# Performance work log

Hardware: AMD Instinct MI355X
Metric: run time of the kernel (lower is better)

The kernel has to match this reference:

```python
import jax, jax.numpy as jnp
import numpy as np

EMBED_DIM = 1024
NUM_HEADS = 16
HEAD_DIM = EMBED_DIM // NUM_HEADS
KERNEL = 3
PAD = KERNEL // 2
B, L = 4, 1024


def conv1d(x, w, b):
    # x: [B, D, L], w: [D_out, D_in, K], b: [D_out]; 'same' padding like nn.Conv1d(padding=K//2)
    y = jax.lax.conv_general_dilated(
        x, w, window_strides=(1,), padding=[(PAD, PAD)],
        dimension_numbers=('NCH', 'OIH', 'NCH'))
    return y + b[None, :, None]


def setup_inputs() -> dict:
    key = jax.random.key(0)
    ks = jax.random.split(key, 12)
    fan = EMBED_DIM * KERNEL
    bound = 1.0 / np.sqrt(fan)
    def wconv(k):
        return jax.random.uniform(k, (EMBED_DIM, EMBED_DIM, KERNEL), jnp.float32, -bound, bound)
    def bconv(k):
        return jax.random.uniform(k, (EMBED_DIM,), jnp.float32, -bound, bound)
    return {
        'query': jax.random.normal(ks[0], (B, L, EMBED_DIM), jnp.float32),
        'key': jax.random.normal(ks[1], (B, L, EMBED_DIM), jnp.float32),
        'value': jax.random.normal(ks[2], (B, L, EMBED_DIM), jnp.float32),
        'key_padding_mask': jax.random.randint(ks[3], (B, L), 0, 2) > 0,
        'attn_mask': jnp.zeros((L, L), jnp.float32),
        'q_w': wconv(ks[4]), 'q_b': bconv(ks[5]),
        'k_w': wconv(ks[6]), 'k_b': bconv(ks[7]),
        'v_w': wconv(ks[8]), 'v_b': bconv(ks[9]),
        'o_w': wconv(ks[10]), 'o_b': bconv(ks[11]),
    }


def reference(query, key, value, key_padding_mask, attn_mask,
              q_w, q_b, k_w, k_b, v_w, v_b, o_w, o_b):
    scale = HEAD_DIM ** -0.5
    # projections: [B, D, L]
    q = conv1d(jnp.swapaxes(query, 1, 2), q_w, q_b)
    k = conv1d(jnp.swapaxes(key, 1, 2), k_w, k_b)
    v = conv1d(jnp.swapaxes(value, 1, 2), v_w, v_b)
    # [B, H, d, L]
    q = q.reshape(B, NUM_HEADS, HEAD_DIM, L)
    k = k.reshape(B, NUM_HEADS, HEAD_DIM, L)
    v = v.reshape(B, NUM_HEADS, HEAD_DIM, L)
    # scores: [B, H, L, L]
    scores = jnp.einsum('bhdi,bhdj->bhij', q, k) * scale
    scores = scores + attn_mask[None, None, :, :]
    scores = jnp.where(key_padding_mask[:, None, None, :], -jnp.inf, scores)
    attn = jax.nn.softmax(scores, axis=-1)  # dropout p=0 (eval) -> identity
    out = jnp.einsum('bhij,bhdj->bhdi', attn, v)  # [B, H, d, L]
    out = out.reshape(B, EMBED_DIM, L)
    out = conv1d(out, o_w, o_b)
    return jnp.swapaxes(out, 1, 2)  # [B, L, D]
```

## Files before the change

kernel.cpp:

```cpp
#include <hip/hip_runtime.h>
#include <math.h>

#define NB 4
#define NL 1024
#define ND 1024
#define NH 16
#define HD 64

typedef __attribute__((ext_vector_type(8))) short bf16x8;
typedef __attribute__((ext_vector_type(4))) float f32x4;

static __device__ __forceinline__ unsigned short f32_to_bf16(float f) {
  unsigned u = __float_as_uint(f);
  u += 0x7FFFu + ((u >> 16) & 1u);
  return (unsigned short)(u >> 16);
}
static __device__ __forceinline__ float bf16_to_f32(unsigned short s) {
  return __uint_as_float(((unsigned)s) << 16);
}
static __device__ __forceinline__ float exp2_f(float x) {
  float r;
  asm("v_exp_f32 %0, %1" : "=v"(r) : "v"(x));
  return r;
}

static __device__ __forceinline__ void split8(float4 a, float4 b, bf16x8* hi, bf16x8* lo) {
  unsigned u[8] = {__float_as_uint(a.x), __float_as_uint(a.y),
                   __float_as_uint(a.z), __float_as_uint(a.w),
                   __float_as_uint(b.x), __float_as_uint(b.y),
                   __float_as_uint(b.z), __float_as_uint(b.w)};
  union { unsigned p[4]; bf16x8 v; } H, L;
#pragma unroll
  for (int p = 0; p < 4; ++p) {
    unsigned u0 = u[2 * p], u1 = u[2 * p + 1];
    H.p[p] = __builtin_amdgcn_perm(u1, u0, 0x07060302u);
    unsigned l0 = __float_as_uint(__uint_as_float(u0) - __uint_as_float(u0 & 0xFFFF0000u));
    unsigned l1 = __float_as_uint(__uint_as_float(u1) - __uint_as_float(u1 & 0xFFFF0000u));
    L.p[p] = __builtin_amdgcn_perm(l1, l0, 0x07060302u);
  }
  *hi = H.v; *lo = L.v;
}

__global__ __launch_bounds__(256) void wcvt_kernel(
    const float* __restrict__ w0, const float* __restrict__ w1,
    const float* __restrict__ w2, const float* __restrict__ w3,
    unsigned short* __restrict__ wb, int* __restrict__ flag)
{
  if (blockIdx.x == 0 && blockIdx.y == 0 && threadIdx.x == 0) flag[0] = 0;
  const int t = blockIdx.y;
  const int o = blockIdx.x;
  const float* w = (t == 0) ? w0 : (t == 1) ? w1 : (t == 2) ? w2 : w3;
  unsigned short* hi = wb + (size_t)t * 6 * (1u << 20);
  unsigned short* lo = hi + 3 * (1u << 20);
  const int tid = threadIdx.x;
  float v[12];
  const float* src = w + (size_t)o * (ND * 3) + tid * 12;
#pragma unroll
  for (int j = 0; j < 3; ++j) {
    float4 f = *(const float4*)(src + j * 4);
    v[j * 4 + 0] = f.x; v[j * 4 + 1] = f.y; v[j * 4 + 2] = f.z; v[j * 4 + 3] = f.w;
  }
#pragma unroll
  for (int k = 0; k < 3; ++k) {
    unsigned short hh[4], ll[4];
#pragma unroll
    for (int ii = 0; ii < 4; ++ii) {
      float x = v[ii * 3 + k];
      unsigned short h = f32_to_bf16(x);
      float r = x - bf16_to_f32(h);
      hh[ii] = h; ll[ii] = f32_to_bf16(r);
    }
    size_t dst = (size_t)k * (ND * ND) + (size_t)o * ND + tid * 4;
    *(ushort4*)&hi[dst] = make_ushort4(hh[0], hh[1], hh[2], hh[3]);
    *(ushort4*)&lo[dst] = make_ushort4(ll[0], ll[1], ll[2], ll[3]);
  }
}

__global__ __launch_bounds__(256) void amask_scan(
    const float* __restrict__ a, int* __restrict__ flag)
{
  size_t i = ((size_t)blockIdx.x * 256 + threadIdx.x) * 4;
  float4 v = *(const float4*)&a[i];
  if (v.x != 0.f || v.y != 0.f || v.z != 0.f || v.w != 0.f) atomicOr(flag, 1);
}

__global__ __launch_bounds__(256, 3) void conv_mfma2(
    const float* X0, const float* X1, const float* X2,
    const unsigned short* __restrict__ wb,
    const float* b0, const float* b1, const float* b2,
    float* Y0, float* Y1, float* Y2, int mode)
{
  __shared__ float Af[128 * 32];
  __shared__ unsigned short Bh[128 * 32];
  __shared__ unsigned short Bl[128 * 32];

  const int tid = threadIdx.x, lane = tid & 63, wave = tid >> 6;
  const int lin = blockIdx.x + 8 * (blockIdx.y + 32 * blockIdx.z);
  const int g = lin & 7, t = lin >> 3;
  const int nb = (g & 3) * 2 + (t & 1);
  const int mb = (g >> 2) * 16 + ((t >> 1) & 15);
  const int z  = t >> 5;
  const int n0 = nb * 128, m0 = mb * 128;
  const int b = m0 >> 10, l0v = m0 & (NL - 1);

  const float* X = (mode == 0) ? (z == 0 ? X0 : (z == 1 ? X1 : X2)) : X0;
  const unsigned short* Wh = (mode == 0) ? wb + (size_t)z * 6 * (1u << 20) : wb;
  const unsigned short* Wl = Wh + 3 * (1u << 20);

  const int wm = (wave >> 1) * 64, wn = (wave & 1) * 64;
  const int mrow = lane & 15, quad = lane >> 4;
  const int r16 = lane >> 2, cs = lane & 3;
  const int src_chunk = (cs - (r16 >> 1)) & 3;
  const int bswz = ((quad + (mrow >> 1)) & 3) * 8;

  f32x4 acc[4][4] = {};

  const int kbeg = (mode == 0) ? 0 : z;
  const int kend = (mode == 0) ? 3 : z + 1;
  for (int koff = kbeg; koff < kend; ++koff) {
    const bool edge_lo = (l0v == 0 && koff == 0);
    const bool edge_hi = (l0v == NL - 128 && koff == 2);
    for (int i0 = 0; i0 < ND; i0 += 32) {
#pragma unroll
      for (int s = 0; s < 2; ++s) {
        const int seg = wave * 2 + s;
        const size_t goff = ((size_t)koff << 20) +
                            (size_t)(n0 + seg * 16 + r16) * ND + i0 + src_chunk * 8;
        __builtin_amdgcn_global_load_lds(
            (const __attribute__((address_space(1))) unsigned int*)(Wh + goff),
            (__attribute__((address_space(3))) unsigned int*)&Bh[seg * 512], 16, 0, 0);
        __builtin_amdgcn_global_load_lds(
            (const __attribute__((address_space(1))) unsigned int*)(Wl + goff),
            (__attribute__((address_space(3))) unsigned int*)&Bl[seg * 512], 16, 0, 0);
      }
#pragma unroll
      for (int j = 0; j < 4; ++j) {
        const int s = (wave * 4 + j) * 64 + lane;
        const int row = s >> 3, sir = s & 7;
        const int chunk = (sir - (row & 7)) & 7;
        int l = l0v + row + koff - 1;
        l = (l < 0) ? 0 : (l > NL - 1 ? NL - 1 : l);
        const float* gp = X + ((size_t)(b << 10) + l) * ND + i0 + chunk * 4;
        __builtin_amdgcn_global_load_lds(
            (const __attribute__((address_space(1))) unsigned int*)gp,
            (__attribute__((address_space(3))) unsigned int*)&Af[(wave * 4 + j) * 256],
            16, 0, 0);
      }
      __syncthreads();
      if (edge_lo || edge_hi) {
        const int er = edge_lo ? 0 : 127;
        if (tid < 8) *(float4*)&Af[er * 32 + tid * 4] = make_float4(0.f, 0.f, 0.f, 0.f);
        __syncthreads();
      }
      bf16x8 ah[4], al[4];
#pragma unroll
      for (int mi = 0; mi < 4; ++mi) {
        const int row = wm + mi * 16 + mrow, r7 = row & 7;
        float4 fa = *(const float4*)&Af[row * 32 + (((quad * 2) + r7) & 7) * 4];
        float4 fb = *(const float4*)&Af[row * 32 + (((quad * 2 + 1) + r7) & 7) * 4];
        split8(fa, fb, &ah[mi], &al[mi]);
      }
#pragma unroll
      for (int ni = 0; ni < 4; ++ni) {
        const int brow = wn + ni * 16 + mrow;
        bf16x8 bh = *(const bf16x8*)&Bh[brow * 32 + bswz];
        bf16x8 bl = *(const bf16x8*)&Bl[brow * 32 + bswz];
#pragma unroll
        for (int mi = 0; mi < 4; ++mi) {
          acc[mi][ni] = __builtin_amdgcn_mfma_f32_16x16x32_bf16(ah[mi], bh, acc[mi][ni], 0, 0, 0);
          acc[mi][ni] = __builtin_amdgcn_mfma_f32_16x16x32_bf16(ah[mi], bl, acc[mi][ni], 0, 0, 0);
          acc[mi][ni] = __builtin_amdgcn_mfma_f32_16x16x32_bf16(al[mi], bh, acc[mi][ni], 0, 0, 0);
        }
      }
      __syncthreads();
    }
  }

  if (mode == 0) {
    const float* bias = (z == 0) ? b0 : (z == 1) ? b1 : b2;
    unsigned short* U = (unsigned short*)Y0;
    const size_t PLs = (size_t)4096 * 1024;
    if (z < 2) {
      unsigned short* Ph = U + (size_t)(2 * z) * PLs;
      unsigned short* Pl = Ph + PLs;
      const float sc = (z == 0) ? 0.18033688011112042f : 1.0f;
#pragma unroll
      for (int ni = 0; ni < 4; ++ni) {
        const int n = n0 + wn + ni * 16 + mrow;
        const float bv = bias[n];
        const int h = n >> 6, dd = n & 63;
        const int bh = b * NH + h;
#pragma unroll
        for (int mi = 0; mi < 4; ++mi) {
          const int mbase = m0 + wm + mi * 16 + quad * 4;
          f32x4 v = acc[mi][ni];
#pragma unroll
          for (int r = 0; r < 4; ++r) {
            const int l = (mbase + r) & (NL - 1);
            const float val = (v[r] + bv) * sc;
            const unsigned u = __float_as_uint(val);
            const unsigned short hh = (unsigned short)(u >> 16);
            const float res = val - __uint_as_float(u & 0xFFFF0000u);
            const unsigned short ll = (unsigned short)(__float_as_uint(res) >> 16);
            const size_t off = ((size_t)bh * NL + l) * HD + dd;
            Ph[off] = hh; Pl[off] = ll;
          }
        }
      }
    } else {
      unsigned short* Pv = U + (size_t)4 * PLs;
#pragma unroll
      for (int ni = 0; ni < 4; ++ni) {
        const int n = n0 + wn + ni * 16 + mrow;
        const float bv = bias[n];
        const int h = n >> 6, dd = n & 63;
        const int bh = b * NH + h;
#pragma unroll
        for (int mi = 0; mi < 4; ++mi) {
          const int mbase = m0 + wm + mi * 16 + quad * 4;
          const int lb = mbase & (NL - 1);
          f32x4 v = acc[mi][ni];
          ushort4 s4 = make_ushort4(f32_to_bf16(v[0] + bv), f32_to_bf16(v[1] + bv),
                                    f32_to_bf16(v[2] + bv), f32_to_bf16(v[3] + bv));
          *(ushort4*)&Pv[((size_t)bh * HD + dd) * NL + lb] = s4;
        }
      }
    }
  } else {
    float* P = Y0 + (size_t)z * ((size_t)NB * NL * ND);
#pragma unroll
    for (int ni = 0; ni < 4; ++ni) {
      const int n = n0 + wn + ni * 16 + mrow;
#pragma unroll
      for (int mi = 0; mi < 4; ++mi) {
        const int mbase = m0 + wm + mi * 16 + quad * 4;
        f32x4 v = acc[mi][ni];
#pragma unroll
        for (int r = 0; r < 4; ++r) {
          const int l = (mbase + r) & (NL - 1);
          P[((size_t)(b << 10) + l) * ND + n] = v[r];
        }
      }
    }
  }
}

__global__ __launch_bounds__(256) void reduce_kernel(
    const float* __restrict__ P, const float* __restrict__ bias, float* __restrict__ out)
{
  const size_t S = (size_t)NB * NL * ND;
  const size_t idx = ((size_t)blockIdx.x * 256 + threadIdx.x) * 4;
  const int n = (int)(idx & (ND - 1));
  float4 p0 = *(const float4*)&P[idx];
  float4 p1 = *(const float4*)&P[idx + S];
  float4 p2 = *(const float4*)&P[idx + 2 * S];
  float4 bv = *(const float4*)&bias[n];
  float4 r;
  r.x = p0.x + p1.x + p2.x + bv.x;
  r.y = p0.y + p1.y + p2.y + bv.y;
  r.z = p0.z + p1.z + p2.z + bv.z;
  r.w = p0.w + p1.w + p2.w + bv.w;
  *(float4*)&out[idx] = r;
}

__global__ __launch_bounds__(256, 3) void attn_mfma(
    const unsigned short* __restrict__ U, const int* __restrict__ kpm,
    const float* __restrict__ amask, const int* __restrict__ aflagp,
    float* __restrict__ AO)
{
  __shared__ __align__(16) unsigned short S[3 * 4096];
  __shared__ __align__(16) float Fm[NL];
  unsigned short* Kh = S;
  unsigned short* Kl = S + 4096;
  unsigned short* Vt = S + 8192;

  const int tid = threadIdx.x, lane = tid & 63, wave = tid >> 6;
  const int c = lane & 15, quad = lane >> 4;
  const int lin = blockIdx.x;
  const int bh = (lin & 7) + 8 * (lin >> 7);
  const int mt = (lin >> 3) & 15;
  const int b = bh >> 4;
  const int m0 = mt * 64;
  const int aflag = *aflagp;
  const int mrow = wave * 16 + c;
  const int gm = m0 + mrow;

  const size_t PLs = (size_t)4096 * 1024;
  const unsigned short* qTh = U;
  const unsigned short* qTl = U + PLs;
  const unsigned short* kTh = U + 2 * PLs;
  const unsigned short* kTl = U + 3 * PLs;
  const unsigned short* vTt = U + 4 * PLs;

  const int srow = lane >> 3;
  const int slot = lane & 7;
  const int chunk = (slot - srow) & 7;

#pragma unroll
  for (int q = 0; q < 4; ++q) {
    const int pl = q >> 1;
    const int i = wave * 2 + (q & 1);
    const int row = i * 8 + srow;
    const unsigned short* src = (pl ? qTl : qTh) +
        ((size_t)bh * NL + m0 + row) * HD + chunk * 8;
    unsigned short* dst = (pl ? Kl : Kh) + i * 512;
    __builtin_amdgcn_global_load_lds(
        (const __attribute__((address_space(1))) unsigned int*)src,
        (__attribute__((address_space(3))) unsigned int*)dst, 16, 0, 0);
  }
  {
    int4 kv = *(const int4*)&kpm[b * NL + tid * 4];
    float4 f;
    f.x = kv.x ? -INFINITY : 0.f;
    f.y = kv.y ? -INFINITY : 0.f;
    f.z = kv.z ? -INFINITY : 0.f;
    f.w = kv.w ? -INFINITY : 0.f;
    *(float4*)&Fm[tid * 4] = f;
  }
  __syncthreads();
  bf16x8 qbh[2], qbl[2];
#pragma unroll
  for (int kb = 0; kb < 2; ++kb) {
    const int cso = ((kb * 4 + quad + mrow) & 7) * 8;
    qbh[kb] = *(const bf16x8*)&Kh[mrow * 64 + cso];
    qbl[kb] = *(const bf16x8*)&Kl[mrow * 64 + cso];
  }

  f32x4 acc[4] = {};
  float m_r = -INFINITY, l_r = 0.0f;

  for (int n0t = 0; n0t < NL; n0t += 64) {
    __syncthreads();

#pragma unroll
    for (int q = 0; q < 6; ++q) {
      const int pl = q >> 1;
      const int i = wave * 2 + (q & 1);
      const int row = i * 8 + srow;
      const unsigned short* src;
      unsigned short* dst;
      if (pl == 0)      { src = kTh + ((size_t)bh * NL + n0t + row) * HD + chunk * 8; dst = Kh + i * 512; }
      else if (pl == 1) { src = kTl + ((size_t)bh * NL + n0t + row) * HD + chunk * 8; dst = Kl + i * 512; }
      else              { src = vTt + ((size_t)bh * HD + row) * NL + n0t + chunk * 8; dst = Vt + i * 512; }
      __builtin_amdgcn_global_load_lds(
          (const __attribute__((address_space(1))) unsigned int*)src,
          (__attribute__((address_space(3))) unsigned int*)dst, 16, 0, 0);
    }

    float mval[4][4];
#pragma unroll
    for (int nf = 0; nf < 4; ++nf) {
      float4 fm = *(const float4*)&Fm[n0t + nf * 16 + quad * 4];
      mval[nf][0] = fm.x; mval[nf][1] = fm.y; mval[nf][2] = fm.z; mval[nf][3] = fm.w;
    }
    if (aflag) {
#pragma unroll
      for (int nf = 0; nf < 4; ++nf)
#pragma unroll
        for (int r = 0; r < 4; ++r) {
          const int gn = n0t + nf * 16 + quad * 4 + r;
          mval[nf][r] += amask[(size_t)gm * NL + gn] * 1.4426950408889634f;
        }
    }
    __syncthreads();

    f32x4 sa[4] = {};
    __builtin_amdgcn_s_setprio(1);
#pragma unroll
    for (int kb = 0; kb < 2; ++kb)
#pragma unroll
      for (int nf = 0; nf < 4; ++nf) {
        const int row = nf * 16 + c;
        const int cso = ((kb * 4 + quad + row) & 7) * 8;
        bf16x8 kah = *(const bf16x8*)&Kh[row * 64 + cso];
        bf16x8 kal = *(const bf16x8*)&Kl[row * 64 + cso];
        sa[nf] = __builtin_amdgcn_mfma_f32_16x16x32_bf16(kah, qbh[kb], sa[nf], 0, 0, 0);
        sa[nf] = __builtin_amdgcn_mfma_f32_16x16x32_bf16(kah, qbl[kb], sa[nf], 0, 0, 0);
        sa[nf] = __builtin_amdgcn_mfma_f32_16x16x32_bf16(kal, qbh[kb], sa[nf], 0, 0, 0);
      }
    __builtin_amdgcn_s_setprio(0);

    float p[4][4];
    float tmax = -INFINITY;
#pragma unroll
    for (int nf = 0; nf < 4; ++nf)
#pragma unroll
      for (int r = 0; r < 4; ++r) {
        float s = sa[nf][r] + mval[nf][r];
        p[nf][r] = s;
        tmax = fmaxf(tmax, s);
      }
    tmax = fmaxf(tmax, __shfl_xor(tmax, 16));
    tmax = fmaxf(tmax, __shfl_xor(tmax, 32));
    float rs = 0.f;
    if (__all(tmax - m_r <= 8.0f)) {
      const float msafe = m_r;
#pragma unroll
      for (int nf = 0; nf < 4; ++nf)
#pragma unroll
        for (int r = 0; r < 4; ++r) {
          float e = exp2_f(p[nf][r] - msafe);
          p[nf][r] = e;
          rs += e;
        }
      rs += __shfl_xor(rs, 16);
      rs += __shfl_xor(rs, 32);
      l_r += rs;
    } else {
      const float newm = fmaxf(m_r, tmax);
      const float msafe = (newm == -INFINITY) ? 0.f : newm;
      const float alpha = exp2_f(m_r - msafe);
#pragma unroll
      for (int nf = 0; nf < 4; ++nf)
#pragma unroll
        for (int r = 0; r < 4; ++r) {
          float e = exp2_f(p[nf][r] - msafe);
          p[nf][r] = e;
          rs += e;
        }
      rs += __shfl_xor(rs, 16);
      rs += __shfl_xor(rs, 32);
      l_r = l_r * alpha + rs;
      m_r = newm;
#pragma unroll
      for (int df = 0; df < 4; ++df) {
        acc[df][0] *= alpha; acc[df][1] *= alpha;
        acc[df][2] *= alpha; acc[df][3] *= alpha;
      }
    }

    unsigned q16[4][2];
#pragma unroll
    for (int nf = 0; nf < 4; ++nf)
#pragma unroll
      for (int w = 0; w < 2; ++w)
        q16[nf][w] = (unsigned)f32_to_bf16(p[nf][2 * w]) |
                     ((unsigned)f32_to_bf16(p[nf][2 * w + 1]) << 16);

#pragma unroll
    for (int kb = 0; kb < 2; ++kb) {
      union { unsigned d[4]; bf16x8 v; } pb;
#pragma unroll
      for (int w = 0; w < 4; ++w) {
        const int addr = ((((quad & 1) * 2 + (w >> 1)) * 16 + c) << 2);
        unsigned v0 = __builtin_amdgcn_ds_bpermute(addr, (int)q16[2 * kb][w & 1]);
        unsigned v1 = __builtin_amdgcn_ds_bpermute(addr, (int)q16[2 * kb + 1][w & 1]);
        pb.d[w] = (quad >> 1) ? v1 : v0;
      }
      __builtin_amdgcn_s_setprio(1);
#pragma unroll
      for (int df = 0; df < 4; ++df) {
        const int row = df * 16 + c;
        const int cso = ((kb * 4 + quad + row) & 7) * 8;
        bf16x8 va = *(const bf16x8*)&Vt[row * 64 + cso];
        acc[df] = __builtin_amdgcn_mfma_f32_16x16x32_bf16(va, pb.v, acc[df], 0, 0, 0);
      }
      __builtin_amdgcn_s_setprio(0);
    }
  }

  __syncthreads();
  const float inv = 1.0f / l_r;
  float* Ob = (float*)S + wave * (16 * 68);
#pragma unroll
  for (int df = 0; df < 4; ++df)
#pragma unroll
    for (int r = 0; r < 4; ++r)
      Ob[c * 68 + df * 16 + quad * 4 + r] = acc[df][r] * inv;
  __syncthreads();
  const int mr2 = lane >> 2, cq2 = lane & 3;
  const int h = bh & 15;
#pragma unroll
  for (int ii = 0; ii < 4; ++ii) {
    const int chunk2 = cq2 * 4 + ii;
    float4 v = *(const float4*)&Ob[mr2 * 68 + chunk2 * 4];
    *(float4*)&AO[((size_t)(b << 10) + (m0 + wave * 16 + mr2)) * ND +
                  h * HD + chunk2 * 4] = v;
  }
}

extern "C" void kernel_launch(void* const* d_in, const int* in_sizes, int n_in,
                              void* d_out, int out_size, void* d_ws, size_t ws_size,
                              hipStream_t stream) {
  (void)in_sizes; (void)n_in; (void)out_size; (void)ws_size;
  const float* query = (const float*)d_in[0];
  const float* key_  = (const float*)d_in[1];
  const float* value = (const float*)d_in[2];
  const int*   kpm   = (const int*)d_in[3];
  const float* amask = (const float*)d_in[4];
  const float* q_w = (const float*)d_in[5];
  const float* q_b = (const float*)d_in[6];
  const float* k_w = (const float*)d_in[7];
  const float* k_b = (const float*)d_in[8];
  const float* v_w = (const float*)d_in[9];
  const float* v_b = (const float*)d_in[10];
  const float* o_w = (const float*)d_in[11];
  const float* o_b = (const float*)d_in[12];
  float* out = (float*)d_out;

  unsigned short* Wb = (unsigned short*)d_ws;
  unsigned short* U  = (unsigned short*)((char*)d_ws + (size_t)50331648);
  float* P  = (float*)((char*)d_ws + (size_t)50331648);
  float* AO = (float*)d_ws;
  int* flag = (int*)d_out;

  wcvt_kernel<<<dim3(1024, 4), 256, 0, stream>>>(q_w, k_w, v_w, o_w, Wb, flag);
  amask_scan<<<1024, 256, 0, stream>>>(amask, flag);
  conv_mfma2<<<dim3(8, 32, 3), 256, 0, stream>>>(
      query, key_, value, Wb, q_b, k_b, v_b, (float*)U, (float*)U, (float*)U, 0);
  attn_mfma<<<1024, 256, 0, stream>>>(U, kpm, amask, flag, AO);
  conv_mfma2<<<dim3(8, 32, 3), 256, 0, stream>>>(
      AO, AO, AO, Wb + (size_t)3 * 6 * (1u << 20), o_b, o_b, o_b, P, P, P, 1);
  reduce_kernel<<<4096, 256, 0, stream>>>(P, o_b, out);
}
```

Before: 501.3 us.

## Double-buffer conv GEMM LDS staging and halve M tile to 64

Restructures the conv projection GEMM into a single flattened k-step loop. The next step's global-to-LDS loads are issued into a second LDS buffer while the current buffer feeds MFMAs, so each step needs one barrier instead of two. The M tile shrinks from 128 to 64 rows, doubling the grid to raise block count. Edge zero-padding now masks the A fragments in registers instead of writing zeros to LDS and syncing. In exchange, each block reuses its weight tile across fewer rows, so weight traffic per output rises, and the doubled LDS footprint may limit occupancy.

```diff
diff --git a/kernel.cpp b/kernel.cpp
--- a/kernel.cpp
+++ b/kernel.cpp
@@ -90,90 +90,103 @@
     const float* b0, const float* b1, const float* b2,
     float* Y0, float* Y1, float* Y2, int mode)
 {
-  __shared__ float Af[128 * 32];
-  __shared__ unsigned short Bh[128 * 32];
-  __shared__ unsigned short Bl[128 * 32];
+  __shared__ __align__(16) unsigned char LDSb[2][24576];
 
   const int tid = threadIdx.x, lane = tid & 63, wave = tid >> 6;
-  const int lin = blockIdx.x + 8 * (blockIdx.y + 32 * blockIdx.z);
+  const int lin = blockIdx.x + 8 * (blockIdx.y + 64 * blockIdx.z);
   const int g = lin & 7, t = lin >> 3;
   const int nb = (g & 3) * 2 + (t & 1);
-  const int mb = (g >> 2) * 16 + ((t >> 1) & 15);
-  const int z  = t >> 5;
-  const int n0 = nb * 128, m0 = mb * 128;
+  const int mb = (g >> 2) * 32 + ((t >> 1) & 31);
+  const int z  = t >> 6;
+  const int n0 = nb * 128, m0 = mb * 64;
   const int b = m0 >> 10, l0v = m0 & (NL - 1);
 
   const float* X = (mode == 0) ? (z == 0 ? X0 : (z == 1 ? X1 : X2)) : X0;
   const unsigned short* Wh = (mode == 0) ? wb + (size_t)z * 6 * (1u << 20) : wb;
   const unsigned short* Wl = Wh + 3 * (1u << 20);
 
-  const int wm = (wave >> 1) * 64, wn = (wave & 1) * 64;
+  const int wm = (wave >> 1) * 32, wn = (wave & 1) * 64;
   const int mrow = lane & 15, quad = lane >> 4;
   const int r16 = lane >> 2, cs = lane & 3;
   const int src_chunk = (cs - (r16 >> 1)) & 3;
   const int bswz = ((quad + (mrow >> 1)) & 3) * 8;
 
-  f32x4 acc[4][4] = {};
-
-  const int kbeg = (mode == 0) ? 0 : z;
-  const int kend = (mode == 0) ? 3 : z + 1;
-  for (int koff = kbeg; koff < kend; ++koff) {
-    const bool edge_lo = (l0v == 0 && koff == 0);
-    const bool edge_hi = (l0v == NL - 128 && koff == 2);
-    for (int i0 = 0; i0 < ND; i0 += 32) {
-#pragma unroll
-      for (int s = 0; s < 2; ++s) {
-        const int seg = wave * 2 + s;
-        const size_t goff = ((size_t)koff << 20) +
-                            (size_t)(n0 + seg * 16 + r16) * ND + i0 + src_chunk * 8;
-        __builtin_amdgcn_global_load_lds(
-            (const __attribute__((address_space(1))) unsigned int*)(Wh + goff),
-            (__attribute__((address_space(3))) unsigned int*)&Bh[seg * 512], 16, 0, 0);
-        __builtin_amdgcn_global_load_lds(
-            (const __attribute__((address_space(1))) unsigned int*)(Wl + goff),
-            (__attribute__((address_space(3))) unsigned int*)&Bl[seg * 512], 16, 0, 0);
-      }
-#pragma unroll
-      for (int j = 0; j < 4; ++j) {
-        const int s = (wave * 4 + j) * 64 + lane;
-        const int row = s >> 3, sir = s & 7;
-        const int chunk = (sir - (row & 7)) & 7;
-        int l = l0v + row + koff - 1;
-        l = (l < 0) ? 0 : (l > NL - 1 ? NL - 1 : l);
-        const float* gp = X + ((size_t)(b << 10) + l) * ND + i0 + chunk * 4;
-        __builtin_amdgcn_global_load_lds(
-            (const __attribute__((address_space(1))) unsigned int*)gp,
-            (__attribute__((address_space(3))) unsigned int*)&Af[(wave * 4 + j) * 256],
-            16, 0, 0);
-      }
-      __syncthreads();
-      if (edge_lo || edge_hi) {
-        const int er = edge_lo ? 0 : 127;
-        if (tid < 8) *(float4*)&Af[er * 32 + tid * 4] = make_float4(0.f, 0.f, 0.f, 0.f);
-        __syncthreads();
-      }
-      bf16x8 ah[4], al[4];
-#pragma unroll
-      for (int mi = 0; mi < 4; ++mi) {
-        const int row = wm + mi * 16 + mrow, r7 = row & 7;
-        float4 fa = *(const float4*)&Af[row * 32 + (((quad * 2) + r7) & 7) * 4];
-        float4 fb = *(const float4*)&Af[row * 32 + (((quad * 2 + 1) + r7) & 7) * 4];
-        split8(fa, fb, &ah[mi], &al[mi]);
-      }
-#pragma unroll
-      for (int ni = 0; ni < 4; ++ni) {
-        const int brow = wn + ni * 16 + mrow;
-        bf16x8 bh = *(const bf16x8*)&Bh[brow * 32 + bswz];
-        bf16x8 bl = *(const bf16x8*)&Bl[brow * 32 + bswz];
-#pragma unroll
-        for (int mi = 0; mi < 4; ++mi) {
-          acc[mi][ni] = __builtin_amdgcn_mfma_f32_16x16x32_bf16(ah[mi], bh, acc[mi][ni], 0, 0, 0);
-          acc[mi][ni] = __builtin_amdgcn_mfma_f32_16x16x32_bf16(ah[mi], bl, acc[mi][ni], 0, 0, 0);
-          acc[mi][ni] = __builtin_amdgcn_mfma_f32_16x16x32_bf16(al[mi], bh, acc[mi][ni], 0, 0, 0);
-        }
-      }
-      __syncthreads();
-    }
+  const int NSTEP = (mode == 0) ? 96 : 32;
+
+  auto stage = [&](int s, int buf) {
+    const int koff = (mode == 0) ? (s >> 5) : z;
+    const int i0 = ((mode == 0) ? (s & 31) : s) << 5;
+    float* AfD = (float*)(LDSb[buf]);
+    unsigned short* BhD = (unsigned short*)(LDSb[buf] + 8192);
+    unsigned short* BlD = (unsigned short*)(LDSb[buf] + 16384);
+#pragma unroll
+    for (int s2 = 0; s2 < 2; ++s2) {
+      const int seg = wave * 2 + s2;
+      const size_t goff = ((size_t)koff << 20) +
+                          (size_t)(n0 + seg * 16 + r16) * ND + i0 + src_chunk * 8;
+      __builtin_amdgcn_global_load_lds(
+          (const __attribute__((address_space(1))) unsigned int*)(Wh + goff),
+          (__attribute__((address_space(3))) unsigned int*)&BhD[seg * 512], 16, 0, 0);
+      __builtin_amdgcn_global_load_lds(
+          (const __attribute__((address_space(1))) unsigned int*)(Wl + goff),
+          (__attribute__((address_space(3))) unsigned int*)&BlD[seg * 512], 16, 0, 0);
+    }
+#pragma unroll
+    for (int j = 0; j < 2; ++j) {
+      const int s2 = (wave * 2 + j) * 64 + lane;
+      const int row = s2 >> 3, sir = s2 & 7;
+      const int chunk = (sir - (row & 7)) & 7;
+      int l = l0v + row + koff - 1;
+      l = (l < 0) ? 0 : (l > NL - 1 ? NL - 1 : l);
+      const float* gp = X + ((size_t)(b << 10) + l) * ND + i0 + chunk * 4;
+      __builtin_amdgcn_global_load_lds(
+          (const __attribute__((address_space(1))) unsigned int*)gp,
+          (__attribute__((address_space(3))) unsigned int*)&AfD[(wave * 2 + j) * 256],
+          16, 0, 0);
+    }
+  };
+
+  f32x4 acc[2][4] = {};
+  const bf16x8 zz = {};
+
+  stage(0, 0);
+  __syncthreads();
+  int cur = 0;
+  for (int s = 0; s < NSTEP; ++s) {
+    if (s + 1 < NSTEP) stage(s + 1, cur ^ 1);
+
+    const int koff = (mode == 0) ? (s >> 5) : z;
+    const bool e_lo = (l0v == 0 && koff == 0);
+    const bool e_hi = (l0v == NL - 64 && koff == 2);
+
+    const float* Af = (const float*)(LDSb[cur]);
+    const unsigned short* Bh = (const unsigned short*)(LDSb[cur] + 8192);
+    const unsigned short* Bl = (const unsigned short*)(LDSb[cur] + 16384);
+
+    bf16x8 ah[2], al[2];
+#pragma unroll
+    for (int mi = 0; mi < 2; ++mi) {
+      const int row = wm + mi * 16 + mrow, r7 = row & 7;
+      float4 fa = *(const float4*)&Af[row * 32 + (((quad * 2) + r7) & 7) * 4];
+      float4 fb = *(const float4*)&Af[row * 32 + (((quad * 2 + 1) + r7) & 7) * 4];
+      split8(fa, fb, &ah[mi], &al[mi]);
+      const bool kill = (e_lo && row == 0) || (e_hi && row == 63);
+      if (kill) { ah[mi] = zz; al[mi] = zz; }
+    }
+#pragma unroll
+    for (int ni = 0; ni < 4; ++ni) {
+      const int brow = wn + ni * 16 + mrow;
+      bf16x8 bh = *(const bf16x8*)&Bh[brow * 32 + bswz];
+      bf16x8 bl = *(const bf16x8*)&Bl[brow * 32 + bswz];
+#pragma unroll
+      for (int mi = 0; mi < 2; ++mi) {
+        acc[mi][ni] = __builtin_amdgcn_mfma_f32_16x16x32_bf16(ah[mi], bh, acc[mi][ni], 0, 0, 0);
+        acc[mi][ni] = __builtin_amdgcn_mfma_f32_16x16x32_bf16(ah[mi], bl, acc[mi][ni], 0, 0, 0);
+        acc[mi][ni] = __builtin_amdgcn_mfma_f32_16x16x32_bf16(al[mi], bh, acc[mi][ni], 0, 0, 0);
+      }
+    }
+    __syncthreads();
+    cur ^= 1;
   }
 
   if (mode == 0) {
@@ -191,7 +204,7 @@
         const int h = n >> 6, dd = n & 63;
         const int bh = b * NH + h;
 #pragma unroll
-        for (int mi = 0; mi < 4; ++mi) {
+        for (int mi = 0; mi < 2; ++mi) {
           const int mbase = m0 + wm + mi * 16 + quad * 4;
           f32x4 v = acc[mi][ni];
 #pragma unroll
@@ -216,7 +229,7 @@
         const int h = n >> 6, dd = n & 63;
         const int bh = b * NH + h;
 #pragma unroll
-        for (int mi = 0; mi < 4; ++mi) {
+        for (int mi = 0; mi < 2; ++mi) {
           const int mbase = m0 + wm + mi * 16 + quad * 4;
           const int lb = mbase & (NL - 1);
           f32x4 v = acc[mi][ni];
@@ -232,7 +245,7 @@
     for (int ni = 0; ni < 4; ++ni) {
       const int n = n0 + wn + ni * 16 + mrow;
 #pragma unroll
-      for (int mi = 0; mi < 4; ++mi) {
+      for (int mi = 0; mi < 2; ++mi) {
         const int mbase = m0 + wm + mi * 16 + quad * 4;
         f32x4 v = acc[mi][ni];
 #pragma unroll
@@ -506,10 +519,10 @@
 
   wcvt_kernel<<<dim3(1024, 4), 256, 0, stream>>>(q_w, k_w, v_w, o_w, Wb, flag);
   amask_scan<<<1024, 256, 0, stream>>>(amask, flag);
-  conv_mfma2<<<dim3(8, 32, 3), 256, 0, stream>>>(
+  conv_mfma2<<<dim3(8, 64, 3), 256, 0, stream>>>(
       query, key_, value, Wb, q_b, k_b, v_b, (float*)U, (float*)U, (float*)U, 0);
   attn_mfma<<<1024, 256, 0, stream>>>(U, kpm, amask, flag, AO);
-  conv_mfma2<<<dim3(8, 32, 3), 256, 0, stream>>>(
+  conv_mfma2<<<dim3(8, 64, 3), 256, 0, stream>>>(
       AO, AO, AO, Wb + (size_t)3 * 6 * (1u << 20), o_b, o_b, o_b, P, P, P, 1);
   reduce_kernel<<<4096, 256, 0, stream>>>(P, o_b, out);
 }
```

New measurement: 576.8 us. +15.1%, slower.
